# Kernel optimization log

Measured on AMD Instinct MI355X. Metric: run time of the kernel, lower is better.

Reference implementation:

```python
import jax, jax.numpy as jnp
import numpy as np

N_NODES = 50000
IN_FEATS, HID_FEATS, OUT_FEATS, HEADS = 128, 32, 64, 4
NEG_SLOPE = 0.2
EPS = 1e-16


def gat_conv(x, src, dst, W, att_src, att_dst, bias, heads, out_ch, concat):
    """PyG-style GATConv. src/dst: [E] (self-loops already included).
    W: [in, heads*out_ch]; att_src/att_dst: [heads, out_ch]; bias: [heads*out_ch] or [out_ch].
    """
    n = x.shape[0]
    xw = (x @ W).reshape(n, heads, out_ch)                     # [N,H,C]
    a_src = (xw * att_src).sum(-1)                             # [N,H]
    a_dst = (xw * att_dst).sum(-1)                             # [N,H]
    e = jax.nn.leaky_relu(a_src[src] + a_dst[dst], NEG_SLOPE)  # [E,H]
    # segment softmax over incoming edges of each destination node
    m = jax.ops.segment_max(e, dst, num_segments=n)
    e = jnp.exp(e - m[dst])
    denom = jax.ops.segment_sum(e, dst, num_segments=n)
    alpha = e / (denom[dst] + EPS)                             # [E,H]
    out = jax.ops.segment_sum(alpha[:, :, None] * xw[src], dst, num_segments=n)  # [N,H,C]
    out = out.reshape(n, heads * out_ch) if concat else out.mean(axis=1)
    return out + bias


def setup_inputs() -> dict:
    key = jax.random.key(0)
    ks = jax.random.split(key, 10)
    E = 1600000
    x = jax.random.normal(ks[0], (N_NODES, IN_FEATS), dtype=jnp.float32)
    edge_index = jax.random.randint(ks[1], (2, E), 0, N_NODES, dtype=jnp.int64)
    s1 = 1.0 / np.sqrt(IN_FEATS)
    W1 = jax.random.uniform(ks[2], (IN_FEATS, HEADS * HID_FEATS), jnp.float32, -s1, s1)
    att_src1 = jax.random.normal(ks[3], (HEADS, HID_FEATS), dtype=jnp.float32) * 0.1
    att_dst1 = jax.random.normal(ks[4], (HEADS, HID_FEATS), dtype=jnp.float32) * 0.1
    b1 = jnp.zeros((HEADS * HID_FEATS,), jnp.float32)
    s2 = 1.0 / np.sqrt(HEADS * HID_FEATS)
    W2 = jax.random.uniform(ks[5], (HEADS * HID_FEATS, OUT_FEATS), jnp.float32, -s2, s2)
    att_src2 = jax.random.normal(ks[6], (1, OUT_FEATS), dtype=jnp.float32) * 0.1
    att_dst2 = jax.random.normal(ks[7], (1, OUT_FEATS), dtype=jnp.float32) * 0.1
    b2 = jnp.zeros((OUT_FEATS,), jnp.float32)
    return {"x": x, "edge_index": edge_index, "W1": W1, "att_src1": att_src1,
            "att_dst1": att_dst1, "b1": b1, "W2": W2, "att_src2": att_src2,
            "att_dst2": att_dst2, "b2": b2}


def reference(x, edge_index, W1, att_src1, att_dst1, b1, W2, att_src2, att_dst2, b2):
    n = x.shape[0]
    loops = jnp.arange(n, dtype=edge_index.dtype)
    src = jnp.concatenate([edge_index[0], loops])
    dst = jnp.concatenate([edge_index[1], loops])
    h = gat_conv(x, src, dst, W1, att_src1, att_dst1, b1, HEADS, HID_FEATS, True)
    h = jax.nn.elu(h)
    h = gat_conv(h, src, dst, W2, att_src2, att_dst2, b2, 1, OUT_FEATS, False)
    return h.mean(axis=0)
```

## Files before the change

kernel.cpp:

```cpp
#include <hip/hip_runtime.h>
#include <math.h>

#define N_NODES 50000
#define SN      N_NODES
#define E_RAW   1600000
#define TE      (E_RAW + N_NODES)
#define TEP     (TE + 16 * N_NODES)
#define F_IN    128
#define H1      4
#define F1      128
#define F2      64
#define NEG_SLOPE 0.2f
#define EPS_F   1e-16f
#define XPAD    136

#define NBINS   196
#define NBLK_A  128
#define EPB     ((TE + NBLK_A - 1) / NBLK_A)
#define MM_BLOCKS (N_NODES / 16)

__device__ __forceinline__ float lrelu(float v) { return v > 0.f ? v : NEG_SLOPE * v; }

typedef float vf2 __attribute__((ext_vector_type(2)));
typedef short short8 __attribute__((ext_vector_type(8)));
typedef float f32x4 __attribute__((ext_vector_type(4)));

__device__ __forceinline__ unsigned short f2bf(float f) {
    unsigned u = __float_as_uint(f);
    return (unsigned short)((u + 0x7fffu + ((u >> 16) & 1u)) >> 16);
}
__device__ __forceinline__ unsigned char f2fp8(float f) {
    int p = __builtin_amdgcn_cvt_pk_fp8_f32(f, f, 0, false);
    return (unsigned char)(p & 0xff);
}
__device__ __forceinline__ vf2 fp8lo(unsigned u) {
    return __builtin_amdgcn_cvt_pk_f32_fp8((int)u, false);
}
__device__ __forceinline__ vf2 fp8hi(unsigned u) {
    return __builtin_amdgcn_cvt_pk_f32_fp8((int)u, true);
}

__global__ __launch_bounds__(256) void k_prep(const float* __restrict__ W1,
                                              const float* __restrict__ W2,
                                              unsigned short* __restrict__ w1t,
                                              unsigned short* __restrict__ w2t,
                                              float* __restrict__ a1s,
                                              float* __restrict__ a2s) {
    int idx = blockIdx.x * 256 + threadIdx.x;
    if (idx < 16384) {
        int c = idx >> 7, k = idx & 127;
        w1t[idx] = f2bf(W1[k * F1 + c]);
    } else {
        int j = idx - 16384;
        int c = j >> 7, k = j & 127;
        w2t[j] = f2bf(W2[k * F2 + c]);
    }
    if (blockIdx.x == 0 && threadIdx.x < H1) a1s[SN * H1 + threadIdx.x] = -1e30f;
    if (blockIdx.x == 0 && threadIdx.x == H1) a2s[SN] = -1e30f;
}

__global__ __launch_bounds__(256) void k_l1_mm_hist(
    const float* __restrict__ x, const unsigned short* __restrict__ w1t,
    const float* __restrict__ atts, const float* __restrict__ attd,
    unsigned char* __restrict__ xwf8, float* __restrict__ a1s, float* __restrict__ a1d,
    const int* __restrict__ ei, int* __restrict__ cnt) {
    __shared__ __align__(16) unsigned short wls[F1 * XPAD];
    __shared__ __align__(16) unsigned short xs[16 * XPAD];
    const int t = threadIdx.x;
    if (blockIdx.x >= MM_BLOCKS) {
        int* hist = (int*)wls;
        const int blk = blockIdx.x - MM_BLOCKS;
        for (int i = t; i < NBINS; i += 256) hist[i] = 0;
        __syncthreads();
        const int e0 = blk * EPB, e1 = min(TE, e0 + EPB);
        for (int e = e0 + t; e < e1; e += 256) {
            int d = (e < E_RAW) ? ei[E_RAW + e] : (e - E_RAW);
            atomicAdd(&hist[d >> 8], 1);
        }
        __syncthreads();
        for (int i = t; i < NBINS; i += 256) cnt[i * NBLK_A + blk] = hist[i];
        return;
    }
    const int n0 = blockIdx.x * 16;
    {
        const float4* src = (const float4*)(x + (size_t)n0 * F_IN);
#pragma unroll
        for (int i = 0; i < 2; ++i) {
            int idx = t + 256 * i;
            float4 v = src[idx];
            int row = idx >> 5;
            int col = (idx & 31) * 4;
            ushort4 o = { f2bf(v.x), f2bf(v.y), f2bf(v.z), f2bf(v.w) };
            *(ushort4*)(xs + row * XPAD + col) = o;
        }
        const uint4* wsrc = (const uint4*)w1t;
#pragma unroll
        for (int i = 0; i < 8; ++i) {
            int idx = t + 256 * i;
            uint4 v = wsrc[idx];
            int row = idx >> 4;
            int col = (idx & 15) * 8;
            *(uint4*)(wls + row * XPAD + col) = v;
        }
    }
    __syncthreads();
    const int w = t >> 6;
    const int lane = t & 63;
    const int quad = lane >> 4;
    const int ncol = lane & 15;
    const int ch0 = w * 32;
    const unsigned short* arow = xs + ncol * XPAD;
    const unsigned short* brow0 = wls + (ch0 + ncol) * XPAD;
    const unsigned short* brow1 = brow0 + 16 * XPAD;
    f32x4 acc0 = {0.f, 0.f, 0.f, 0.f}, acc1 = {0.f, 0.f, 0.f, 0.f};
#pragma unroll
    for (int s = 0; s < 4; ++s) {
        int kb = s * 32 + quad * 8;
        short8 a  = *(const short8*)(arow + kb);
        short8 b0 = *(const short8*)(brow0 + kb);
        short8 b1 = *(const short8*)(brow1 + kb);
        acc0 = __builtin_amdgcn_mfma_f32_16x16x32_bf16(a, b0, acc0, 0, 0, 0);
        acc1 = __builtin_amdgcn_mfma_f32_16x16x32_bf16(a, b1, acc1, 0, 0, 0);
    }
    const int ch = ch0 + ncol;
    const float as0 = atts[ch], as1 = atts[ch + 16];
    const float ad0 = attd[ch], ad1 = attd[ch + 16];
#pragma unroll
    for (int reg = 0; reg < 4; ++reg) {
        const int n = n0 + quad * 4 + reg;
        float v0 = acc0[reg], v1 = acc1[reg];
        xwf8[(size_t)n * F1 + ch] = f2fp8(v0);
        xwf8[(size_t)n * F1 + ch + 16] = f2fp8(v1);
        float ps = fmaf(v0, as0, v1 * as1);
        float pd = fmaf(v0, ad0, v1 * ad1);
#pragma unroll
        for (int off = 1; off < 16; off <<= 1) {
            ps += __shfl_xor(ps, off);
            pd += __shfl_xor(pd, off);
        }
        if (ncol == 0) {
            a1s[n * H1 + w] = ps;
            a1d[n * H1 + w] = pd;
        }
    }
}

__global__ __launch_bounds__(64) void k_btot(int* __restrict__ cnt, int* __restrict__ btot) {
    const int bin = blockIdx.x, lane = threadIdx.x;
    int c0 = cnt[bin * NBLK_A + 2 * lane];
    int c1 = cnt[bin * NBLK_A + 2 * lane + 1];
    int s = c0 + c1;
    int incl = s;
#pragma unroll
    for (int off = 1; off < 64; off <<= 1) {
        int u = __shfl_up(incl, off, 64);
        if (lane >= off) incl += u;
    }
    int excl = incl - s;
    cnt[bin * NBLK_A + 2 * lane] = excl;
    cnt[bin * NBLK_A + 2 * lane + 1] = excl + c0;
    if (lane == 63) btot[bin] = incl;
}

__global__ __launch_bounds__(64) void k_bstart(const int* __restrict__ btot,
                                               int* __restrict__ bstart) {
    const int lane = threadIdx.x;
    int v[4]; int s = 0;
#pragma unroll
    for (int j = 0; j < 4; ++j) {
        int i = 4 * lane + j;
        v[j] = (i < NBINS) ? btot[i] : 0;
        s += v[j];
    }
    int incl = s;
#pragma unroll
    for (int off = 1; off < 64; off <<= 1) {
        int u = __shfl_up(incl, off, 64);
        if (lane >= off) incl += u;
    }
    int run = incl - s;
#pragma unroll
    for (int j = 0; j < 4; ++j) {
        int i = 4 * lane + j;
        if (i < NBINS) bstart[i] = run;
        run += v[j];
    }
    if (lane == 63) bstart[NBINS] = TE;
}

__global__ __launch_bounds__(256) void k_scatter_coarse(const int* __restrict__ ei,
                                                        const int* __restrict__ cnt,
                                                        const int* __restrict__ bstart,
                                                        unsigned* __restrict__ cbuf) {
    __shared__ int cur[NBINS];
    const int t = threadIdx.x, blk = blockIdx.x;
    for (int i = t; i < NBINS; i += 256) cur[i] = cnt[i * NBLK_A + blk] + bstart[i];
    __syncthreads();
    const int e0 = blk * EPB, e1 = min(TE, e0 + EPB);
    for (int e = e0 + t; e < e1; e += 256) {
        int s, d;
        if (e < E_RAW) { s = ei[e]; d = ei[E_RAW + e]; }
        else { s = e - E_RAW; d = s; }
        int pos = atomicAdd(&cur[d >> 8], 1);
        cbuf[pos] = ((unsigned)(d & 255) << 16) | (unsigned)s;
    }
}

__global__ __launch_bounds__(256) void k_fine_hist(const unsigned* __restrict__ cbuf,
                                                   const int* __restrict__ bstart,
                                                   int* __restrict__ deg) {
    __shared__ int hist[256];
    const int t = threadIdx.x, b = blockIdx.x;
    hist[t] = 0;
    __syncthreads();
    const int i0 = bstart[b], i1 = bstart[b + 1];
    for (int i = i0 + t; i < i1; i += 256) atomicAdd(&hist[cbuf[i] >> 16], 1);
    __syncthreads();
    const int d = b * 256 + t;
    if (d < N_NODES) deg[d] = hist[t];
}

__global__ __launch_bounds__(1024) void k_scan1(const int* __restrict__ deg,
                                                int* __restrict__ incl, int* __restrict__ bsum) {
    int t = threadIdx.x, g = blockIdx.x;
    int idx = g * 1024 + t;
    int v = (idx < N_NODES) ? ((deg[idx] + 15) & ~15) : 0;
    int lane = t & 63, w = t >> 6;
#pragma unroll
    for (int off = 1; off < 64; off <<= 1) {
        int u = __shfl_up(v, off, 64);
        if (lane >= off) v += u;
    }
    __shared__ int ws[16];
    if (lane == 63) ws[w] = v;
    __syncthreads();
    if (w == 0 && lane < 16) {
        int s = ws[lane];
#pragma unroll
        for (int off = 1; off < 16; off <<= 1) {
            int u = __shfl_up(s, off, 16);
            if (lane >= off) s += u;
        }
        ws[lane] = s;
    }
    __syncthreads();
    if (w > 0) v += ws[w - 1];
    if (idx < N_NODES) incl[idx] = v;
    if (t == 1023) bsum[g] = v;
}

__global__ void k_scan2(int* __restrict__ bsum, int nblk) {
    int t = threadIdx.x;
    int v = (t < nblk) ? bsum[t] : 0;
#pragma unroll
    for (int off = 1; off < 64; off <<= 1) {
        int u = __shfl_up(v, off, 64);
        if (t >= off) v += u;
    }
    if (t < nblk) bsum[t] = v;
}

__global__ __launch_bounds__(1024) void k_scan3(const int* __restrict__ incl,
                                                const int* __restrict__ bsum,
                                                int* __restrict__ rowstart) {
    int idx = blockIdx.x * 1024 + threadIdx.x;
    if (idx >= N_NODES) return;
    int off = (blockIdx.x > 0) ? bsum[blockIdx.x - 1] : 0;
    rowstart[idx + 1] = incl[idx] + off;
    if (idx == 0) rowstart[0] = 0;
}

__global__ __launch_bounds__(256) void k_build_csr(const unsigned* __restrict__ cbuf,
                                                   const int* __restrict__ bstart,
                                                   const int* __restrict__ rowstart,
                                                   const int* __restrict__ deg,
                                                   int* __restrict__ csr) {
    __shared__ int cur[256];
    const int t = threadIdx.x, b = blockIdx.x;
    const int d = b * 256 + t;
    cur[t] = (d < N_NODES) ? rowstart[d] : 0;
    __syncthreads();
    const int i0 = bstart[b], i1 = bstart[b + 1];
    for (int i = i0 + t; i < i1; i += 256) {
        unsigned v = cbuf[i];
        int pos = atomicAdd(&cur[v >> 16], 1);
        csr[pos] = (int)(v & 0xffffu);
    }
    __syncthreads();
    if (d < N_NODES) {
        const int pend = rowstart[d] + ((deg[d] + 15) & ~15);
        for (int i = cur[t]; i < pend; ++i) csr[i] = SN;
    }
}

__global__ __launch_bounds__(256) void k_l1_gather(
    const int* __restrict__ rowstart, const int* __restrict__ csr,
    const int* __restrict__ deg, const float* __restrict__ a1s,
    const float* __restrict__ a1d, const unsigned* __restrict__ xwu,
    const float* __restrict__ b1, float* __restrict__ h1) {
    const int lane = threadIdx.x & 63;
    const int wid = threadIdx.x >> 6;
    const int n = blockIdx.x * 4 + wid;
    if (n >= N_NODES) return;
    const int rs = rowstart[n];
    const int nb16 = (deg[n] + 15) >> 4;
    const int half = lane >> 5;
    const int sub = lane & 31;
    const int h = sub >> 3;
    const float adh = a1d[n * H1 + h];
    const int4* c4 = (const int4*)(csr + rs);
    const int eoff = half * 8 + (sub & 7);
    const int wbase = half * 32 + (h << 3);
    float den = 0.f, f0 = 0.f, f1 = 0.f, f2 = 0.f, f3 = 0.f;
    for (int b = 0; b < nb16; ++b) {
        const int i0 = 4 * b + 2 * half;
        int4 sA = c4[i0], sB = c4[i0 + 1];
        int se = csr[rs + 16 * b + eoff];
        unsigned u0 = xwu[sA.x * 32 + sub], u1 = xwu[sA.y * 32 + sub];
        unsigned u2 = xwu[sA.z * 32 + sub], u3 = xwu[sA.w * 32 + sub];
        unsigned u4 = xwu[sB.x * 32 + sub], u5 = xwu[sB.y * 32 + sub];
        unsigned u6 = xwu[sB.z * 32 + sub], u7 = xwu[sB.w * 32 + sub];
        float we = __expf(lrelu(a1s[se * H1 + h] + adh));
        float w0 = __shfl(we, wbase + 0), w1 = __shfl(we, wbase + 1);
        float w2 = __shfl(we, wbase + 2), w3 = __shfl(we, wbase + 3);
        float w4 = __shfl(we, wbase + 4), w5 = __shfl(we, wbase + 5);
        float w6 = __shfl(we, wbase + 6), w7 = __shfl(we, wbase + 7);
        den += ((w0 + w1) + (w2 + w3)) + ((w4 + w5) + (w6 + w7));
        vf2 l0 = fp8lo(u0), v0 = fp8hi(u0);
        f0 = fmaf(w0, l0.x, f0); f1 = fmaf(w0, l0.y, f1);
        f2 = fmaf(w0, v0.x, f2); f3 = fmaf(w0, v0.y, f3);
        vf2 l1 = fp8lo(u1), v1 = fp8hi(u1);
        f0 = fmaf(w1, l1.x, f0); f1 = fmaf(w1, l1.y, f1);
        f2 = fmaf(w1, v1.x, f2); f3 = fmaf(w1, v1.y, f3);
        vf2 l2 = fp8lo(u2), v2 = fp8hi(u2);
        f0 = fmaf(w2, l2.x, f0); f1 = fmaf(w2, l2.y, f1);
        f2 = fmaf(w2, v2.x, f2); f3 = fmaf(w2, v2.y, f3);
        vf2 l3 = fp8lo(u3), v3 = fp8hi(u3);
        f0 = fmaf(w3, l3.x, f0); f1 = fmaf(w3, l3.y, f1);
        f2 = fmaf(w3, v3.x, f2); f3 = fmaf(w3, v3.y, f3);
        vf2 l4 = fp8lo(u4), v4 = fp8hi(u4);
        f0 = fmaf(w4, l4.x, f0); f1 = fmaf(w4, l4.y, f1);
        f2 = fmaf(w4, v4.x, f2); f3 = fmaf(w4, v4.y, f3);
        vf2 l5 = fp8lo(u5), v5 = fp8hi(u5);
        f0 = fmaf(w5, l5.x, f0); f1 = fmaf(w5, l5.y, f1);
        f2 = fmaf(w5, v5.x, f2); f3 = fmaf(w5, v5.y, f3);
        vf2 l6 = fp8lo(u6), v6 = fp8hi(u6);
        f0 = fmaf(w6, l6.x, f0); f1 = fmaf(w6, l6.y, f1);
        f2 = fmaf(w6, v6.x, f2); f3 = fmaf(w6, v6.y, f3);
        vf2 l7 = fp8lo(u7), v7 = fp8hi(u7);
        f0 = fmaf(w7, l7.x, f0); f1 = fmaf(w7, l7.y, f1);
        f2 = fmaf(w7, v7.x, f2); f3 = fmaf(w7, v7.y, f3);
    }
    f0 += __shfl_xor(f0, 32);
    f1 += __shfl_xor(f1, 32);
    f2 += __shfl_xor(f2, 32);
    f3 += __shfl_xor(f3, 32);
    den += __shfl_xor(den, 32);
    if (half == 0) {
        const float inv = 1.f / (den + EPS_F);
        float4 bb = ((const float4*)b1)[sub];
        float o0 = fmaf(f0, inv, bb.x);
        float o1 = fmaf(f1, inv, bb.y);
        float o2 = fmaf(f2, inv, bb.z);
        float o3 = fmaf(f3, inv, bb.w);
        o0 = o0 > 0.f ? o0 : expm1f(o0);
        o1 = o1 > 0.f ? o1 : expm1f(o1);
        o2 = o2 > 0.f ? o2 : expm1f(o2);
        o3 = o3 > 0.f ? o3 : expm1f(o3);
        ((float4*)h1)[(size_t)n * 32 + sub] = make_float4(o0, o1, o2, o3);
    }
}

__global__ __launch_bounds__(256) void k_l2_mm(
    const float* __restrict__ h1, const unsigned short* __restrict__ w2t,
    const float* __restrict__ atts, const float* __restrict__ attd,
    unsigned char* __restrict__ xwf8, float* __restrict__ a2s, float* __restrict__ a2d) {
    __shared__ __align__(16) unsigned short wls[F2 * XPAD];
    __shared__ __align__(16) unsigned short xs[16 * XPAD];
    __shared__ float parts[16][4], partd[16][4];
    const int t = threadIdx.x;
    const int n0 = blockIdx.x * 16;
    {
        const float4* src = (const float4*)(h1 + (size_t)n0 * F1);
#pragma unroll
        for (int i = 0; i < 2; ++i) {
            int idx = t + 256 * i;
            float4 v = src[idx];
            int row = idx >> 5;
            int col = (idx & 31) * 4;
            ushort4 o = { f2bf(v.x), f2bf(v.y), f2bf(v.z), f2bf(v.w) };
            *(ushort4*)(xs + row * XPAD + col) = o;
        }
        const uint4* wsrc = (const uint4*)w2t;
#pragma unroll
        for (int i = 0; i < 4; ++i) {
            int idx = t + 256 * i;
            uint4 v = wsrc[idx];
            int row = idx >> 4;
            int col = (idx & 15) * 8;
            *(uint4*)(wls + row * XPAD + col) = v;
        }
    }
    __syncthreads();
    const int w = t >> 6;
    const int lane = t & 63;
    const int quad = lane >> 4;
    const int ncol = lane & 15;
    const int ch0 = w * 16;
    const unsigned short* arow = xs + ncol * XPAD;
    const unsigned short* brow = wls + (ch0 + ncol) * XPAD;
    f32x4 acc = {0.f, 0.f, 0.f, 0.f};
#pragma unroll
    for (int s = 0; s < 4; ++s) {
        int kb = s * 32 + quad * 8;
        short8 a = *(const short8*)(arow + kb);
        short8 b = *(const short8*)(brow + kb);
        acc = __builtin_amdgcn_mfma_f32_16x16x32_bf16(a, b, acc, 0, 0, 0);
    }
    const int ch = ch0 + ncol;
    const float asv = atts[ch], adv = attd[ch];
#pragma unroll
    for (int reg = 0; reg < 4; ++reg) {
        const int m = quad * 4 + reg;
        float v = acc[reg];
        xwf8[(size_t)(n0 + m) * F2 + ch] = f2fp8(v);
        float ps = v * asv, pd = v * adv;
#pragma unroll
        for (int off = 1; off < 16; off <<= 1) {
            ps += __shfl_xor(ps, off);
            pd += __shfl_xor(pd, off);
        }
        if (ncol == 0) { parts[m][w] = ps; partd[m][w] = pd; }
    }
    __syncthreads();
    if (t < 16) {
        a2s[n0 + t] = (parts[t][0] + parts[t][1]) + (parts[t][2] + parts[t][3]);
        a2d[n0 + t] = (partd[t][0] + partd[t][1]) + (partd[t][2] + partd[t][3]);
    }
}

__global__ __launch_bounds__(256) void k_l2_gather(
    const int* __restrict__ rowstart, const int* __restrict__ csr,
    const int* __restrict__ deg, const float* __restrict__ a2s,
    const float* __restrict__ a2d, const unsigned* __restrict__ xwu,
    float* __restrict__ h2) {
    const int lane = threadIdx.x & 63;
    const int wid = threadIdx.x >> 6;
    const int n = blockIdx.x * 4 + wid;
    if (n >= N_NODES) return;
    const int rs = rowstart[n];
    const int nb16 = (deg[n] + 15) >> 4;
    const int q = lane >> 4;
    const int sub = lane & 15;
    const float adv = a2d[n];
    const int4* c4 = (const int4*)(csr + rs);
    float den = 0.f, f0 = 0.f, f1 = 0.f, f2 = 0.f, f3 = 0.f;
    for (int b = 0; b < nb16; ++b) {
        int4 s4 = c4[4 * b + q];
        int se = csr[rs + 16 * b + sub];
        unsigned u0 = xwu[s4.x * 16 + sub], u1 = xwu[s4.y * 16 + sub];
        unsigned u2 = xwu[s4.z * 16 + sub], u3 = xwu[s4.w * 16 + sub];
        float we = __expf(lrelu(a2s[se] + adv));
        float w0 = __shfl(we, 4 * q + 0), w1 = __shfl(we, 4 * q + 1);
        float w2 = __shfl(we, 4 * q + 2), w3 = __shfl(we, 4 * q + 3);
        den += (w0 + w1) + (w2 + w3);
        vf2 l0 = fp8lo(u0), v0 = fp8hi(u0);
        f0 = fmaf(w0, l0.x, f0); f1 = fmaf(w0, l0.y, f1);
        f2 = fmaf(w0, v0.x, f2); f3 = fmaf(w0, v0.y, f3);
        vf2 l1 = fp8lo(u1), v1 = fp8hi(u1);
        f0 = fmaf(w1, l1.x, f0); f1 = fmaf(w1, l1.y, f1);
        f2 = fmaf(w1, v1.x, f2); f3 = fmaf(w1, v1.y, f3);
        vf2 l2 = fp8lo(u2), v2 = fp8hi(u2);
        f0 = fmaf(w2, l2.x, f0); f1 = fmaf(w2, l2.y, f1);
        f2 = fmaf(w2, v2.x, f2); f3 = fmaf(w2, v2.y, f3);
        vf2 l3 = fp8lo(u3), v3 = fp8hi(u3);
        f0 = fmaf(w3, l3.x, f0); f1 = fmaf(w3, l3.y, f1);
        f2 = fmaf(w3, v3.x, f2); f3 = fmaf(w3, v3.y, f3);
    }
#pragma unroll
    for (int off = 16; off <= 32; off <<= 1) {
        f0 += __shfl_xor(f0, off);
        f1 += __shfl_xor(f1, off);
        f2 += __shfl_xor(f2, off);
        f3 += __shfl_xor(f3, off);
        den += __shfl_xor(den, off);
    }
    if (lane < 16) {
        const float inv = 1.f / (den + EPS_F);
        ((float4*)h2)[(size_t)n * 16 + sub] =
            make_float4(f0 * inv, f1 * inv, f2 * inv, f3 * inv);
    }
}

#define MEAN_BLOCKS 256
__global__ __launch_bounds__(256) void k_mean(const float* __restrict__ h2,
                                              double* __restrict__ accum) {
    const int t = threadIdx.x;
    const int c = t & 63;
    double acc = 0.0;
    const size_t total = (size_t)N_NODES * F2;
    for (size_t idx = (size_t)blockIdx.x * 256 + t; idx < total; idx += (size_t)MEAN_BLOCKS * 256)
        acc += (double)h2[idx];
    __shared__ double red[256];
    red[t] = acc;
    __syncthreads();
    if (t < 64) {
        double v = red[t] + red[t + 64] + red[t + 128] + red[t + 192];
        atomicAdd(&accum[c], v);
    }
}

__global__ void k_final(const double* __restrict__ accum, const float* __restrict__ b2,
                        float* __restrict__ out) {
    int t = threadIdx.x;
    if (t < F2) out[t] = (float)(accum[t] * (1.0 / (double)N_NODES)) + b2[t];
}

extern "C" void kernel_launch(void* const* d_in, const int* in_sizes, int n_in,
                              void* d_out, int out_size, void* d_ws, size_t ws_size,
                              hipStream_t stream) {
    (void)in_sizes; (void)n_in; (void)out_size; (void)ws_size;
    const float* x   = (const float*)d_in[0];
    const int*   ei  = (const int*)d_in[1];
    const float* W1  = (const float*)d_in[2];
    const float* as1 = (const float*)d_in[3];
    const float* ad1 = (const float*)d_in[4];
    const float* b1  = (const float*)d_in[5];
    const float* W2  = (const float*)d_in[6];
    const float* as2 = (const float*)d_in[7];
    const float* ad2 = (const float*)d_in[8];
    const float* b2  = (const float*)d_in[9];
    float* out = (float*)d_out;

    char* ws = (char*)d_ws;
    size_t off = 0;
    auto alloc = [&](size_t bytes) -> void* {
        void* p = ws + off;
        off += (bytes + 255) & ~(size_t)255;
        return p;
    };
    unsigned char*  xw1f8 = (unsigned char*)alloc((size_t)(N_NODES + 1) * F1);
    float* h1       = (float*)alloc((size_t)N_NODES * F1 * 4);
    unsigned char*  xw2f8 = (unsigned char*)alloc((size_t)(N_NODES + 1) * F2);
    float* h2       = (float*)alloc((size_t)N_NODES * F2 * 4);
    unsigned short* w1t = (unsigned short*)alloc((size_t)F1 * F1 * 2);
    unsigned short* w2t = (unsigned short*)alloc((size_t)F2 * F1 * 2);
    float* a1s      = (float*)alloc((size_t)(N_NODES + 1) * H1 * 4);
    float* a1d      = (float*)alloc((size_t)N_NODES * H1 * 4);
    float* a2s      = (float*)alloc((size_t)(N_NODES + 1) * 4);
    float* a2d      = (float*)alloc((size_t)N_NODES * 4);
    int*   deg      = (int*)alloc((size_t)N_NODES * 4);
    unsigned* cbuf  = (unsigned*)alloc((size_t)TE * 4);
    int*   cnt      = (int*)alloc((size_t)NBINS * NBLK_A * 4);
    int*   btot     = (int*)alloc((size_t)NBINS * 4);
    int*   bstart   = (int*)alloc((size_t)(NBINS + 1) * 4);
    int*   rowstart = (int*)alloc((size_t)(N_NODES + 1) * 4);
    int*   csr      = (int*)alloc((size_t)TEP * 4);
    int*   incl     = (int*)alloc((size_t)N_NODES * 4);
    int*   bsum     = (int*)alloc(64 * 4);
    double* accum   = (double*)alloc(F2 * 8);

    const int nscan = (N_NODES + 1023) / 1024;
    const int nwave4 = (N_NODES + 3) / 4;

    hipMemsetAsync(accum, 0, F2 * 8, stream);
    k_prep<<<96, 256, 0, stream>>>(W1, W2, w1t, w2t, a1s, a2s);
    k_l1_mm_hist<<<MM_BLOCKS + NBLK_A, 256, 0, stream>>>(x, w1t, as1, ad1, xw1f8, a1s, a1d, ei, cnt);
    k_btot<<<NBINS, 64, 0, stream>>>(cnt, btot);
    k_bstart<<<1, 64, 0, stream>>>(btot, bstart);
    k_scatter_coarse<<<NBLK_A, 256, 0, stream>>>(ei, cnt, bstart, cbuf);
    k_fine_hist<<<NBINS, 256, 0, stream>>>(cbuf, bstart, deg);
    k_scan1<<<nscan, 1024, 0, stream>>>(deg, incl, bsum);
    k_scan2<<<1, 64, 0, stream>>>(bsum, nscan);
    k_scan3<<<nscan, 1024, 0, stream>>>(incl, bsum, rowstart);
    k_build_csr<<<NBINS, 256, 0, stream>>>(cbuf, bstart, rowstart, deg, csr);
    k_l1_gather<<<nwave4, 256, 0, stream>>>(rowstart, csr, deg, a1s, a1d,
                                            (const unsigned*)xw1f8, b1, h1);
    k_l2_mm<<<MM_BLOCKS, 256, 0, stream>>>(h1, w2t, as2, ad2, xw2f8, a2s, a2d);
    k_l2_gather<<<nwave4, 256, 0, stream>>>(rowstart, csr, deg, a2s, a2d,
                                            (const unsigned*)xw2f8, h2);
    k_mean<<<MEAN_BLOCKS, 256, 0, stream>>>(h2, accum);
    k_final<<<1, 64, 0, stream>>>(accum, b2, out);
}
```

Measured before the change: 268.3 us.

## Widen gather loads to 8 fp8 per lane, use packed FMA, store h1 as bf16

Both gather kernels now load 8 fp8 features per lane with uint2 loads instead of 4, so fewer lanes cover a row and more edges are handled in parallel per wave. Accumulation uses packed two-wide float FMAs. Layer-1 output is written as bf16 instead of fp32, which halves h1 traffic and removes the fp32-to-bf16 conversion from the layer-2 matmul load. The cost is a wider cross-lane reduction at the end and different per-lane register pressure.

```diff
diff --git a/kernel.cpp b/kernel.cpp
--- a/kernel.cpp
+++ b/kernel.cpp
@@ -28,6 +28,9 @@
 __device__ __forceinline__ unsigned short f2bf(float f) {
     unsigned u = __float_as_uint(f);
     return (unsigned short)((u + 0x7fffu + ((u >> 16) & 1u)) >> 16);
+}
+__device__ __forceinline__ unsigned bfpack(float lo, float hi) {
+    return ((unsigned)f2bf(lo)) | (((unsigned)f2bf(hi)) << 16);
 }
 __device__ __forceinline__ unsigned char f2fp8(float f) {
     int p = __builtin_amdgcn_cvt_pk_fp8_f32(f, f, 0, false);
@@ -296,83 +299,83 @@
 __global__ __launch_bounds__(256) void k_l1_gather(
     const int* __restrict__ rowstart, const int* __restrict__ csr,
     const int* __restrict__ deg, const float* __restrict__ a1s,
-    const float* __restrict__ a1d, const unsigned* __restrict__ xwu,
-    const float* __restrict__ b1, float* __restrict__ h1) {
+    const float* __restrict__ a1d, const uint2* __restrict__ xwv,
+    const float* __restrict__ b1, unsigned* __restrict__ h1bf) {
     const int lane = threadIdx.x & 63;
     const int wid = threadIdx.x >> 6;
     const int n = blockIdx.x * 4 + wid;
     if (n >= N_NODES) return;
     const int rs = rowstart[n];
     const int nb16 = (deg[n] + 15) >> 4;
-    const int half = lane >> 5;
-    const int sub = lane & 31;
-    const int h = sub >> 3;
-    const float adh = a1d[n * H1 + h];
+    const int q = lane >> 4;
+    const int sub = lane & 15;
+    const float adh = a1d[n * H1 + q];
+    const int wbase = (sub >> 2) * 16 + 4 * q;
     const int4* c4 = (const int4*)(csr + rs);
-    const int eoff = half * 8 + (sub & 7);
-    const int wbase = half * 32 + (h << 3);
-    float den = 0.f, f0 = 0.f, f1 = 0.f, f2 = 0.f, f3 = 0.f;
+    vf2 f01 = {0.f, 0.f}, f23 = {0.f, 0.f}, f45 = {0.f, 0.f}, f67 = {0.f, 0.f};
+    float den = 0.f;
     for (int b = 0; b < nb16; ++b) {
-        const int i0 = 4 * b + 2 * half;
-        int4 sA = c4[i0], sB = c4[i0 + 1];
-        int se = csr[rs + 16 * b + eoff];
-        unsigned u0 = xwu[sA.x * 32 + sub], u1 = xwu[sA.y * 32 + sub];
-        unsigned u2 = xwu[sA.z * 32 + sub], u3 = xwu[sA.w * 32 + sub];
-        unsigned u4 = xwu[sB.x * 32 + sub], u5 = xwu[sB.y * 32 + sub];
-        unsigned u6 = xwu[sB.z * 32 + sub], u7 = xwu[sB.w * 32 + sub];
-        float we = __expf(lrelu(a1s[se * H1 + h] + adh));
+        int4 sQ = c4[4 * b + q];
+        int se = csr[rs + 16 * b + sub];
+        uint2 u0 = xwv[sQ.x * 16 + sub], u1 = xwv[sQ.y * 16 + sub];
+        uint2 u2 = xwv[sQ.z * 16 + sub], u3 = xwv[sQ.w * 16 + sub];
+        float we = __expf(lrelu(a1s[se * H1 + q] + adh));
         float w0 = __shfl(we, wbase + 0), w1 = __shfl(we, wbase + 1);
         float w2 = __shfl(we, wbase + 2), w3 = __shfl(we, wbase + 3);
-        float w4 = __shfl(we, wbase + 4), w5 = __shfl(we, wbase + 5);
-        float w6 = __shfl(we, wbase + 6), w7 = __shfl(we, wbase + 7);
-        den += ((w0 + w1) + (w2 + w3)) + ((w4 + w5) + (w6 + w7));
-        vf2 l0 = fp8lo(u0), v0 = fp8hi(u0);
-        f0 = fmaf(w0, l0.x, f0); f1 = fmaf(w0, l0.y, f1);
-        f2 = fmaf(w0, v0.x, f2); f3 = fmaf(w0, v0.y, f3);
-        vf2 l1 = fp8lo(u1), v1 = fp8hi(u1);
-        f0 = fmaf(w1, l1.x, f0); f1 = fmaf(w1, l1.y, f1);
-        f2 = fmaf(w1, v1.x, f2); f3 = fmaf(w1, v1.y, f3);
-        vf2 l2 = fp8lo(u2), v2 = fp8hi(u2);
-        f0 = fmaf(w2, l2.x, f0); f1 = fmaf(w2, l2.y, f1);
-        f2 = fmaf(w2, v2.x, f2); f3 = fmaf(w2, v2.y, f3);
-        vf2 l3 = fp8lo(u3), v3 = fp8hi(u3);
-        f0 = fmaf(w3, l3.x, f0); f1 = fmaf(w3, l3.y, f1);
-        f2 = fmaf(w3, v3.x, f2); f3 = fmaf(w3, v3.y, f3);
-        vf2 l4 = fp8lo(u4), v4 = fp8hi(u4);
-        f0 = fmaf(w4, l4.x, f0); f1 = fmaf(w4, l4.y, f1);
-        f2 = fmaf(w4, v4.x, f2); f3 = fmaf(w4, v4.y, f3);
-        vf2 l5 = fp8lo(u5), v5 = fp8hi(u5);
-        f0 = fmaf(w5, l5.x, f0); f1 = fmaf(w5, l5.y, f1);
-        f2 = fmaf(w5, v5.x, f2); f3 = fmaf(w5, v5.y, f3);
-        vf2 l6 = fp8lo(u6), v6 = fp8hi(u6);
-        f0 = fmaf(w6, l6.x, f0); f1 = fmaf(w6, l6.y, f1);
-        f2 = fmaf(w6, v6.x, f2); f3 = fmaf(w6, v6.y, f3);
-        vf2 l7 = fp8lo(u7), v7 = fp8hi(u7);
-        f0 = fmaf(w7, l7.x, f0); f1 = fmaf(w7, l7.y, f1);
-        f2 = fmaf(w7, v7.x, f2); f3 = fmaf(w7, v7.y, f3);
-    }
-    f0 += __shfl_xor(f0, 32);
-    f1 += __shfl_xor(f1, 32);
-    f2 += __shfl_xor(f2, 32);
-    f3 += __shfl_xor(f3, 32);
-    den += __shfl_xor(den, 32);
-    if (half == 0) {
+        den += (w0 + w1) + (w2 + w3);
+        vf2 wv;
+        wv[0] = w0; wv[1] = w0;
+        f01 = __builtin_elementwise_fma(wv, fp8lo(u0.x), f01);
+        f23 = __builtin_elementwise_fma(wv, fp8hi(u0.x), f23);
+        f45 = __builtin_elementwise_fma(wv, fp8lo(u0.y), f45);
+        f67 = __builtin_elementwise_fma(wv, fp8hi(u0.y), f67);
+        wv[0] = w1; wv[1] = w1;
+        f01 = __builtin_elementwise_fma(wv, fp8lo(u1.x), f01);
+        f23 = __builtin_elementwise_fma(wv, fp8hi(u1.x), f23);
+        f45 = __builtin_elementwise_fma(wv, fp8lo(u1.y), f45);
+        f67 = __builtin_elementwise_fma(wv, fp8hi(u1.y), f67);
+        wv[0] = w2; wv[1] = w2;
+        f01 = __builtin_elementwise_fma(wv, fp8lo(u2.x), f01);
+        f23 = __builtin_elementwise_fma(wv, fp8hi(u2.x), f23);
+        f45 = __builtin_elementwise_fma(wv, fp8lo(u2.y), f45);
+        f67 = __builtin_elementwise_fma(wv, fp8hi(u2.y), f67);
+        wv[0] = w3; wv[1] = w3;
+        f01 = __builtin_elementwise_fma(wv, fp8lo(u3.x), f01);
+        f23 = __builtin_elementwise_fma(wv, fp8hi(u3.x), f23);
+        f45 = __builtin_elementwise_fma(wv, fp8lo(u3.y), f45);
+        f67 = __builtin_elementwise_fma(wv, fp8hi(u3.y), f67);
+    }
+#pragma unroll
+    for (int off = 16; off <= 32; off <<= 1) {
+        f01[0] += __shfl_xor(f01[0], off); f01[1] += __shfl_xor(f01[1], off);
+        f23[0] += __shfl_xor(f23[0], off); f23[1] += __shfl_xor(f23[1], off);
+        f45[0] += __shfl_xor(f45[0], off); f45[1] += __shfl_xor(f45[1], off);
+        f67[0] += __shfl_xor(f67[0], off); f67[1] += __shfl_xor(f67[1], off);
+        den += __shfl_xor(den, off);
+    }
+    if (q == 0) {
         const float inv = 1.f / (den + EPS_F);
-        float4 bb = ((const float4*)b1)[sub];
-        float o0 = fmaf(f0, inv, bb.x);
-        float o1 = fmaf(f1, inv, bb.y);
-        float o2 = fmaf(f2, inv, bb.z);
-        float o3 = fmaf(f3, inv, bb.w);
+        float4 b0 = ((const float4*)b1)[2 * sub];
+        float4 b1v = ((const float4*)b1)[2 * sub + 1];
+        float o0 = fmaf(f01[0], inv, b0.x), o1 = fmaf(f01[1], inv, b0.y);
+        float o2 = fmaf(f23[0], inv, b0.z), o3 = fmaf(f23[1], inv, b0.w);
+        float o4 = fmaf(f45[0], inv, b1v.x), o5 = fmaf(f45[1], inv, b1v.y);
+        float o6 = fmaf(f67[0], inv, b1v.z), o7 = fmaf(f67[1], inv, b1v.w);
         o0 = o0 > 0.f ? o0 : expm1f(o0);
         o1 = o1 > 0.f ? o1 : expm1f(o1);
         o2 = o2 > 0.f ? o2 : expm1f(o2);
         o3 = o3 > 0.f ? o3 : expm1f(o3);
-        ((float4*)h1)[(size_t)n * 32 + sub] = make_float4(o0, o1, o2, o3);
+        o4 = o4 > 0.f ? o4 : expm1f(o4);
+        o5 = o5 > 0.f ? o5 : expm1f(o5);
+        o6 = o6 > 0.f ? o6 : expm1f(o6);
+        o7 = o7 > 0.f ? o7 : expm1f(o7);
+        uint4 pk = { bfpack(o0, o1), bfpack(o2, o3), bfpack(o4, o5), bfpack(o6, o7) };
+        ((uint4*)h1bf)[(size_t)n * 16 + sub] = pk;
     }
 }
 
 __global__ __launch_bounds__(256) void k_l2_mm(
-    const float* __restrict__ h1, const unsigned short* __restrict__ w2t,
+    const unsigned* __restrict__ h1bf, const unsigned short* __restrict__ w2t,
     const float* __restrict__ atts, const float* __restrict__ attd,
     unsigned char* __restrict__ xwf8, float* __restrict__ a2s, float* __restrict__ a2d) {
     __shared__ __align__(16) unsigned short wls[F2 * XPAD];
@@ -381,24 +384,19 @@
     const int t = threadIdx.x;
     const int n0 = blockIdx.x * 16;
     {
-        const float4* src = (const float4*)(h1 + (size_t)n0 * F1);
-#pragma unroll
-        for (int i = 0; i < 2; ++i) {
-            int idx = t + 256 * i;
-            float4 v = src[idx];
-            int row = idx >> 5;
-            int col = (idx & 31) * 4;
-            ushort4 o = { f2bf(v.x), f2bf(v.y), f2bf(v.z), f2bf(v.w) };
-            *(ushort4*)(xs + row * XPAD + col) = o;
-        }
+        const uint4* src = (const uint4*)(h1bf + (size_t)n0 * 64);
+        uint4 v = src[t];
+        int row = t >> 4;
+        int col = (t & 15) * 8;
+        *(uint4*)(xs + row * XPAD + col) = v;
         const uint4* wsrc = (const uint4*)w2t;
 #pragma unroll
         for (int i = 0; i < 4; ++i) {
             int idx = t + 256 * i;
-            uint4 v = wsrc[idx];
-            int row = idx >> 4;
-            int col = (idx & 15) * 8;
-            *(uint4*)(wls + row * XPAD + col) = v;
+            uint4 wv = wsrc[idx];
+            int wrow = idx >> 4;
+            int wcol = (idx & 15) * 8;
+            *(uint4*)(wls + wrow * XPAD + wcol) = wv;
         }
     }
     __syncthreads();
@@ -442,7 +440,7 @@
 __global__ __launch_bounds__(256) void k_l2_gather(
     const int* __restrict__ rowstart, const int* __restrict__ csr,
     const int* __restrict__ deg, const float* __restrict__ a2s,
-    const float* __restrict__ a2d, const unsigned* __restrict__ xwu,
+    const float* __restrict__ a2d, const uint2* __restrict__ xwv,
     float* __restrict__ h2) {
     const int lane = threadIdx.x & 63;
     const int wid = threadIdx.x >> 6;
@@ -450,45 +448,45 @@
     if (n >= N_NODES) return;
     const int rs = rowstart[n];
     const int nb16 = (deg[n] + 15) >> 4;
-    const int q = lane >> 4;
-    const int sub = lane & 15;
+    const int g = lane >> 3;
+    const int sub = lane & 7;
     const float adv = a2d[n];
-    const int4* c4 = (const int4*)(csr + rs);
-    float den = 0.f, f0 = 0.f, f1 = 0.f, f2 = 0.f, f3 = 0.f;
+    const int2* c2 = (const int2*)(csr + rs);
+    vf2 f01 = {0.f, 0.f}, f23 = {0.f, 0.f}, f45 = {0.f, 0.f}, f67 = {0.f, 0.f};
+    float den = 0.f;
     for (int b = 0; b < nb16; ++b) {
-        int4 s4 = c4[4 * b + q];
-        int se = csr[rs + 16 * b + sub];
-        unsigned u0 = xwu[s4.x * 16 + sub], u1 = xwu[s4.y * 16 + sub];
-        unsigned u2 = xwu[s4.z * 16 + sub], u3 = xwu[s4.w * 16 + sub];
+        int2 sG = c2[8 * b + g];
+        int se = csr[rs + 16 * b + (lane & 15)];
+        uint2 u0 = xwv[sG.x * 8 + sub], u1 = xwv[sG.y * 8 + sub];
         float we = __expf(lrelu(a2s[se] + adv));
-        float w0 = __shfl(we, 4 * q + 0), w1 = __shfl(we, 4 * q + 1);
-        float w2 = __shfl(we, 4 * q + 2), w3 = __shfl(we, 4 * q + 3);
-        den += (w0 + w1) + (w2 + w3);
-        vf2 l0 = fp8lo(u0), v0 = fp8hi(u0);
-        f0 = fmaf(w0, l0.x, f0); f1 = fmaf(w0, l0.y, f1);
-        f2 = fmaf(w0, v0.x, f2); f3 = fmaf(w0, v0.y, f3);
-        vf2 l1 = fp8lo(u1), v1 = fp8hi(u1);
-        f0 = fmaf(w1, l1.x, f0); f1 = fmaf(w1, l1.y, f1);
-        f2 = fmaf(w1, v1.x, f2); f3 = fmaf(w1, v1.y, f3);
-        vf2 l2 = fp8lo(u2), v2 = fp8hi(u2);
-        f0 = fmaf(w2, l2.x, f0); f1 = fmaf(w2, l2.y, f1);
-        f2 = fmaf(w2, v2.x, f2); f3 = fmaf(w2, v2.y, f3);
-        vf2 l3 = fp8lo(u3), v3 = fp8hi(u3);
-        f0 = fmaf(w3, l3.x, f0); f1 = fmaf(w3, l3.y, f1);
-        f2 = fmaf(w3, v3.x, f2); f3 = fmaf(w3, v3.y, f3);
-    }
-#pragma unroll
-    for (int off = 16; off <= 32; off <<= 1) {
-        f0 += __shfl_xor(f0, off);
-        f1 += __shfl_xor(f1, off);
-        f2 += __shfl_xor(f2, off);
-        f3 += __shfl_xor(f3, off);
+        float w0 = __shfl(we, 2 * g), w1 = __shfl(we, 2 * g + 1);
+        den += w0 + w1;
+        vf2 wv;
+        wv[0] = w0; wv[1] = w0;
+        f01 = __builtin_elementwise_fma(wv, fp8lo(u0.x), f01);
+        f23 = __builtin_elementwise_fma(wv, fp8hi(u0.x), f23);
+        f45 = __builtin_elementwise_fma(wv, fp8lo(u0.y), f45);
+        f67 = __builtin_elementwise_fma(wv, fp8hi(u0.y), f67);
+        wv[0] = w1; wv[1] = w1;
+        f01 = __builtin_elementwise_fma(wv, fp8lo(u1.x), f01);
+        f23 = __builtin_elementwise_fma(wv, fp8hi(u1.x), f23);
+        f45 = __builtin_elementwise_fma(wv, fp8lo(u1.y), f45);
+        f67 = __builtin_elementwise_fma(wv, fp8hi(u1.y), f67);
+    }
+#pragma unroll
+    for (int off = 8; off <= 32; off <<= 1) {
+        f01[0] += __shfl_xor(f01[0], off); f01[1] += __shfl_xor(f01[1], off);
+        f23[0] += __shfl_xor(f23[0], off); f23[1] += __shfl_xor(f23[1], off);
+        f45[0] += __shfl_xor(f45[0], off); f45[1] += __shfl_xor(f45[1], off);
+        f67[0] += __shfl_xor(f67[0], off); f67[1] += __shfl_xor(f67[1], off);
         den += __shfl_xor(den, off);
     }
-    if (lane < 16) {
+    if (lane < 8) {
         const float inv = 1.f / (den + EPS_F);
-        ((float4*)h2)[(size_t)n * 16 + sub] =
-            make_float4(f0 * inv, f1 * inv, f2 * inv, f3 * inv);
+        float4 o0 = make_float4(f01[0] * inv, f01[1] * inv, f23[0] * inv, f23[1] * inv);
+        float4 o1 = make_float4(f45[0] * inv, f45[1] * inv, f67[0] * inv, f67[1] * inv);
+        ((float4*)h2)[(size_t)n * 16 + 2 * sub] = o0;
+        ((float4*)h2)[(size_t)n * 16 + 2 * sub + 1] = o1;
     }
 }
 
@@ -540,7 +538,7 @@
         return p;
     };
     unsigned char*  xw1f8 = (unsigned char*)alloc((size_t)(N_NODES + 1) * F1);
-    float* h1       = (float*)alloc((size_t)N_NODES * F1 * 4);
+    unsigned* h1bf  = (unsigned*)alloc((size_t)N_NODES * F1 * 2);
     unsigned char*  xw2f8 = (unsigned char*)alloc((size_t)(N_NODES + 1) * F2);
     float* h2       = (float*)alloc((size_t)N_NODES * F2 * 4);
     unsigned short* w1t = (unsigned short*)alloc((size_t)F1 * F1 * 2);
@@ -575,10 +573,10 @@
     k_scan3<<<nscan, 1024, 0, stream>>>(incl, bsum, rowstart);
     k_build_csr<<<NBINS, 256, 0, stream>>>(cbuf, bstart, rowstart, deg, csr);
     k_l1_gather<<<nwave4, 256, 0, stream>>>(rowstart, csr, deg, a1s, a1d,
-                                            (const unsigned*)xw1f8, b1, h1);
-    k_l2_mm<<<MM_BLOCKS, 256, 0, stream>>>(h1, w2t, as2, ad2, xw2f8, a2s, a2d);
+                                            (const uint2*)xw1f8, b1, h1bf);
+    k_l2_mm<<<MM_BLOCKS, 256, 0, stream>>>(h1bf, w2t, as2, ad2, xw2f8, a2s, a2d);
     k_l2_gather<<<nwave4, 256, 0, stream>>>(rowstart, csr, deg, a2s, a2d,
-                                            (const unsigned*)xw2f8, h2);
+                                            (const uint2*)xw2f8, h2);
     k_mean<<<MEAN_BLOCKS, 256, 0, stream>>>(h2, accum);
     k_final<<<1, 64, 0, stream>>>(accum, b2, out);
 }
```

New measurement: 280.0 us. 1.04x slower.
